# Kernel optimization log

Measured on AMD Instinct MI355X. Metric: run time of the kernel, lower is better.

Reference implementation:

```python
import jax, jax.numpy as jnp
import numpy as np

B, S, D = 2, 2048, 1024
H, HD = 16, 64  # head_dim = D // H
NEG = -9.0e15


def setup_inputs() -> dict:
    key = jax.random.key(0)
    ks = jax.random.split(key, 6)
    # xavier-uniform-like init for projections
    lim_qkv = float(np.sqrt(6.0 / (D + 3 * D)))
    lim_o = float(np.sqrt(6.0 / (D + D)))
    x = jax.random.normal(ks[0], (B, S, D), dtype=jnp.float32)
    qkv_w = jax.random.uniform(ks[1], (3 * D, D), minval=-lim_qkv, maxval=lim_qkv, dtype=jnp.float32)
    qkv_b = jnp.zeros((3 * D,), dtype=jnp.float32)
    o_w = jax.random.uniform(ks[2], (D, D), minval=-lim_o, maxval=lim_o, dtype=jnp.float32)
    o_b = jnp.zeros((D,), dtype=jnp.float32)
    # per-head thresholds ~ Uniform(0, 2/S): mean softmax prob is 1/S, so
    # roughly half the heads prune aggressively, half keep most entries.
    thresholds = jax.random.uniform(ks[3], (H,), dtype=jnp.float32) * (2.0 / S)
    return {"x": x, "thresholds": thresholds, "qkv_w": qkv_w, "qkv_b": qkv_b,
            "o_w": o_w, "o_b": o_b}


def reference(x, thresholds, qkv_w, qkv_b, o_w, o_b):
    # qkv projection: [B,S,3D] -> [B,S,H,3*HD] -> [B,H,S,3*HD]
    qkv = jnp.einsum('bsd,ed->bse', x, qkv_w) + qkv_b
    qkv = qkv.reshape(B, S, H, 3 * HD).transpose(0, 2, 1, 3)
    q, k, v = jnp.split(qkv, 3, axis=-1)  # each [B,H,S,HD]

    scale = 1.0 / jnp.sqrt(jnp.asarray(HD, dtype=q.dtype))
    attn_logits = jnp.einsum('bhqd,bhkd->bhqk', q, k) * scale  # [B,H,S,S]

    # first softmax only to build threshold mask (per-head threshold)
    att1 = jax.nn.softmax(attn_logits, axis=-1)
    mask = att1 > thresholds[None, :, None, None]

    # second, masked softmax
    masked_logits = jnp.where(mask, attn_logits, jnp.asarray(NEG, attn_logits.dtype))
    attention = jax.nn.softmax(masked_logits, axis=-1)

    values = jnp.einsum('bhqk,bhkd->bhqd', attention, v)  # [B,H,S,HD]
    values = values.transpose(0, 2, 1, 3).reshape(B, S, D)
    o = jnp.einsum('bsd,ed->bse', values, o_w) + o_b
    return o
```

## Files before the change

kernel.cpp:

```cpp
#include <hip/hip_runtime.h>
#include <math.h>

#define BATCH 2
#define S_LEN 2048
#define DMODEL 1024
#define NH 16
#define HDIM 64
#define SCALE 0.125f
#define KC 0.18033688011112042f

typedef short bf16x8 __attribute__((ext_vector_type(8)));
typedef _Float16 f16x8 __attribute__((ext_vector_type(8)));
typedef float f32x4 __attribute__((ext_vector_type(4)));
typedef unsigned short u16;
typedef unsigned short u16x4 __attribute__((ext_vector_type(4)));
#define MFMA(a, b, c) __builtin_amdgcn_mfma_f32_16x16x32_bf16(a, b, c, 0, 0, 0)
#define MFMA16(a, b, c) __builtin_amdgcn_mfma_f32_16x16x32_f16(a, b, c, 0, 0, 0)

static __device__ __forceinline__ float bf2f(u16 u) {
  return __uint_as_float(((unsigned int)u) << 16);
}
static __device__ __forceinline__ u16 f2h_bits(float a) {
  _Float16 h = (_Float16)a;
  return *(u16*)&h;
}

static __device__ __forceinline__ void split_bf16(float a, u16& hi, u16& lo) {
  unsigned int u = __float_as_uint(a);
  unsigned int r = (u + 0x7fffu + ((u >> 16) & 1u)) >> 16;
  hi = (u16)r;
  float res = a - __uint_as_float(r << 16);
  unsigned int u2 = __float_as_uint(res);
  lo = (u16)((u2 + 0x7fffu + ((u2 >> 16) & 1u)) >> 16);
}

static __device__ __forceinline__ float qredsum(float v) {
#pragma unroll
  for (int off = 8; off >= 1; off >>= 1) v += __shfl_xor(v, off, 16);
  return v;
}

static __device__ __forceinline__ void async_ld16(u16* lds, const u16* g) {
  __builtin_amdgcn_global_load_lds(
      (const __attribute__((address_space(1))) void*)(const void*)g,
      (__attribute__((address_space(3))) void*)(void*)lds, 16, 0, 0);
}

__global__ __launch_bounds__(256) void split_pair_kernel(
    const float* __restrict__ in, u16* __restrict__ hi, u16* __restrict__ lo,
    int n) {
  int idx = (blockIdx.x * 256 + threadIdx.x) * 4;
  if (idx >= n) return;
  float4 v = *(const float4*)(in + idx);
  u16 h0, h1, h2, h3, l0, l1, l2, l3;
  split_bf16(v.x, h0, l0);
  split_bf16(v.y, h1, l1);
  split_bf16(v.z, h2, l2);
  split_bf16(v.w, h3, l3);
  u16x4 h = {h0, h1, h2, h3};
  u16x4 l = {l0, l1, l2, l3};
  *(u16x4*)(hi + idx) = h;
  *(u16x4*)(lo + idx) = l;
}

__global__ __launch_bounds__(256) void qkv_gemm_mfma(
    const u16* __restrict__ xh, const u16* __restrict__ xl,
    const u16* __restrict__ wh, const u16* __restrict__ wl,
    const float* __restrict__ bias, u16* __restrict__ Qhi,
    u16* __restrict__ Qlo, u16* __restrict__ Khi, u16* __restrict__ Klo,
    u16* __restrict__ Vt) {
  __shared__ __align__(16) u16 Ah[4096], Al[4096], Bh[4096], Bl[4096];
  const int tid = threadIdx.x;
  const int w = tid >> 6, lane = tid & 63;
  const int m = lane & 15, quad = lane >> 4;
  const int wm = w >> 1, wn = w & 1;
  const int m0 = blockIdx.x * 128, n0 = blockIdx.y * 128;
  const int rl = lane >> 2, bp = lane & 3;
  const int sst = (rl >> 1) & 3;
  const int sa = (quad ^ ((m >> 1) & 3)) * 8;

  f32x4 acc[4][4];
  const f32x4 vzero = {0.f, 0.f, 0.f, 0.f};
#pragma unroll
  for (int mt = 0; mt < 4; ++mt)
#pragma unroll
    for (int nt = 0; nt < 4; ++nt) acc[mt][nt] = vzero;

  for (int k0 = 0; k0 < DMODEL; k0 += 32) {
#pragma unroll
    for (int i = 0; i < 2; ++i) {
      int cc = w * 2 + i;
      int row = cc * 16 + rl;
      int gofs = k0 + ((bp ^ sst) << 3);
      async_ld16(&Ah[cc * 512], xh + (size_t)(m0 + row) * DMODEL + gofs);
      async_ld16(&Al[cc * 512], xl + (size_t)(m0 + row) * DMODEL + gofs);
      async_ld16(&Bh[cc * 512], wh + (size_t)(n0 + row) * DMODEL + gofs);
      async_ld16(&Bl[cc * 512], wl + (size_t)(n0 + row) * DMODEL + gofs);
    }
    __syncthreads();
    bf16x8 afh[4], afl[4], bfh[4], bfl[4];
#pragma unroll
    for (int t = 0; t < 4; ++t) {
      int ra = (wm * 64 + t * 16 + m) * 32 + sa;
      afh[t] = *(const bf16x8*)&Ah[ra];
      afl[t] = *(const bf16x8*)&Al[ra];
      int rb = (wn * 64 + t * 16 + m) * 32 + sa;
      bfh[t] = *(const bf16x8*)&Bh[rb];
      bfl[t] = *(const bf16x8*)&Bl[rb];
    }
#pragma unroll
    for (int mt = 0; mt < 4; ++mt)
#pragma unroll
      for (int nt = 0; nt < 4; ++nt) {
        acc[mt][nt] = MFMA(afh[mt], bfh[nt], acc[mt][nt]);
        acc[mt][nt] = MFMA(afh[mt], bfl[nt], acc[mt][nt]);
        acc[mt][nt] = MFMA(afl[mt], bfh[nt], acc[mt][nt]);
      }
    __syncthreads();
  }
#pragma unroll
  for (int mt = 0; mt < 4; ++mt) {
#pragma unroll
    for (int rg = 0; rg < 4; ++rg) {
      int grow = m0 + wm * 64 + mt * 16 + quad * 4 + rg;
      int bb = grow >> 11, s = grow & (S_LEN - 1);
#pragma unroll
      for (int nt = 0; nt < 4; ++nt) {
        int e = n0 + wn * 64 + nt * 16 + m;
        float val = acc[mt][nt][rg] + bias[e];
        int h = e / 192;
        int r = e - h * 192;
        int d = r & 63;
        int bh = bb * NH + h;
        if (r < 64) {
          u16 hi, lo;
          split_bf16(val, hi, lo);
          int off = (bh * S_LEN + s) * HDIM + d;
          Qhi[off] = hi; Qlo[off] = lo;
        } else if (r < 128) {
          u16 hi, lo;
          split_bf16(val, hi, lo);
          int off = (bh * S_LEN + s) * HDIM + d;
          Khi[off] = hi; Klo[off] = lo;
        } else {
          Vt[(bh * HDIM + d) * S_LEN + s] = f2h_bits(val);
        }
      }
    }
  }
}

__global__ __launch_bounds__(256) void o_gemm_mfma(
    const u16* __restrict__ valh, const u16* __restrict__ vall,
    const float* __restrict__ ow, const float* __restrict__ bias,
    float* __restrict__ out) {
  __shared__ __align__(16) u16 Ah[4096], Al[4096], Bh[4096], Bl[4096];
  const int tid = threadIdx.x;
  const int w = tid >> 6, lane = tid & 63;
  const int m = lane & 15, quad = lane >> 4;
  const int wm = w >> 1, wn = w & 1;
  const int m0 = blockIdx.x * 128, n0 = blockIdx.y * 128;
  const int rl = lane >> 2, bp = lane & 3;
  const int sst = (rl >> 1) & 3;
  const int sa = (quad ^ ((m >> 1) & 3)) * 8;
  const int rB = tid >> 1, hf = tid & 1;
  const int sB = (rB >> 1) & 3;

  f32x4 acc[4][4];
  const f32x4 vzero = {0.f, 0.f, 0.f, 0.f};
#pragma unroll
  for (int mt = 0; mt < 4; ++mt)
#pragma unroll
    for (int nt = 0; nt < 4; ++nt) acc[mt][nt] = vzero;

  for (int k0 = 0; k0 < DMODEL; k0 += 32) {
#pragma unroll
    for (int i = 0; i < 2; ++i) {
      int cc = w * 2 + i;
      int row = cc * 16 + rl;
      int gofs = k0 + ((bp ^ sst) << 3);
      async_ld16(&Ah[cc * 512], valh + (size_t)(m0 + row) * DMODEL + gofs);
      async_ld16(&Al[cc * 512], vall + (size_t)(m0 + row) * DMODEL + gofs);
    }
    {
      const float* src = ow + (size_t)(n0 + rB) * DMODEL + k0 + hf * 16;
      float tmp[16];
      *(float4*)&tmp[0] = *(const float4*)(src);
      *(float4*)&tmp[4] = *(const float4*)(src + 4);
      *(float4*)&tmp[8] = *(const float4*)(src + 8);
      *(float4*)&tmp[12] = *(const float4*)(src + 12);
      u16 hbuf[16], lbuf[16];
#pragma unroll
      for (int ii = 0; ii < 16; ++ii) split_bf16(tmp[ii], hbuf[ii], lbuf[ii]);
#pragma unroll
      for (int j = 0; j < 2; ++j) {
        int bs = ((2 * hf + j) ^ sB) * 8;
        bf16x8 hv, lv;
#pragma unroll
        for (int q2 = 0; q2 < 8; ++q2) {
          hv[q2] = (short)hbuf[j * 8 + q2];
          lv[q2] = (short)lbuf[j * 8 + q2];
        }
        *(bf16x8*)&Bh[rB * 32 + bs] = hv;
        *(bf16x8*)&Bl[rB * 32 + bs] = lv;
      }
    }
    __syncthreads();
    bf16x8 afh[4], afl[4], bfh[4], bfl[4];
#pragma unroll
    for (int t = 0; t < 4; ++t) {
      int ra = (wm * 64 + t * 16 + m) * 32 + sa;
      afh[t] = *(const bf16x8*)&Ah[ra];
      afl[t] = *(const bf16x8*)&Al[ra];
      int rb = (wn * 64 + t * 16 + m) * 32 + sa;
      bfh[t] = *(const bf16x8*)&Bh[rb];
      bfl[t] = *(const bf16x8*)&Bl[rb];
    }
#pragma unroll
    for (int mt = 0; mt < 4; ++mt)
#pragma unroll
      for (int nt = 0; nt < 4; ++nt) {
        acc[mt][nt] = MFMA(afh[mt], bfh[nt], acc[mt][nt]);
        acc[mt][nt] = MFMA(afh[mt], bfl[nt], acc[mt][nt]);
        acc[mt][nt] = MFMA(afl[mt], bfh[nt], acc[mt][nt]);
      }
    __syncthreads();
  }
#pragma unroll
  for (int mt = 0; mt < 4; ++mt) {
#pragma unroll
    for (int rg = 0; rg < 4; ++rg) {
      int grow = m0 + wm * 64 + mt * 16 + quad * 4 + rg;
#pragma unroll
      for (int nt = 0; nt < 4; ++nt) {
        int e = n0 + wn * 64 + nt * 16 + m;
        out[(size_t)grow * DMODEL + e] = acc[mt][nt][rg] + bias[e];
      }
    }
  }
}

__global__ __launch_bounds__(256) void vsum_kernel(const u16* __restrict__ Vt,
                                                   float* __restrict__ vsum) {
  const int bh = blockIdx.x;
  const int tid = threadIdx.x;
  const int d = tid >> 2, part = tid & 3;
  int base = (bh * HDIM + d) * S_LEN + part * 512;
  float s = 0.f;
  for (int k = 0; k < 512; k += 8) {
    f16x8 vv = *(const f16x8*)(Vt + base + k);
#pragma unroll
    for (int j = 0; j < 8; ++j) s += (float)vv[j];
  }
  __shared__ float red[64][4];
  red[d][part] = s;
  __syncthreads();
  if (part == 0)
    vsum[bh * HDIM + d] = red[d][0] + red[d][1] + red[d][2] + red[d][3];
}

__global__ __launch_bounds__(256) void attn_mfma_kernel(
    const u16* __restrict__ Qhi, const u16* __restrict__ Qlo,
    const u16* __restrict__ Khi, const u16* __restrict__ Klo,
    const u16* __restrict__ Vt, const float* __restrict__ thr,
    const float* __restrict__ vsum, u16* __restrict__ valh,
    u16* __restrict__ vall) {
  const int blk = blockIdx.x;
  const int qt = blk & 31, bh = blk >> 5;
  const int h = bh & (NH - 1), bb = bh >> 4;
  const int tid = threadIdx.x;
  const int w = tid >> 6, lane = tid & 63;
  const int m = lane & 15, quad = lane >> 4;
  const int rsub = lane >> 3;
  const int bsw = (lane & 7) ^ rsub;

  __shared__ __align__(16) u16 Kh_s[2][4096];
  __shared__ __align__(16) u16 Kl_s[2][4096];
  __shared__ __align__(16) u16 Vs_s[4096];
  __shared__ __align__(16) u16 Pf_s[4][16][64];

  const int qoff = (bh * S_LEN + qt * 64 + w * 16 + m) * HDIM + quad * 8;
  const bf16x8 aQh0 = *(const bf16x8*)(Qhi + qoff);
  const bf16x8 aQh1 = *(const bf16x8*)(Qhi + qoff + 32);
  const bf16x8 aQl0 = *(const bf16x8*)(Qlo + qoff);
  const bf16x8 aQl1 = *(const bf16x8*)(Qlo + qoff + 32);

  const u16* KhT = Khi + bh * S_LEN * HDIM;
  const u16* KlT = Klo + bh * S_LEN * HDIM;
  const u16* VtT = Vt + bh * HDIM * S_LEN;
  const float th = thr[h];

  const int s0 = (quad ^ (m & 7)) * 8;
  const int s1 = ((4 + quad) ^ (m & 7)) * 8;

  float Zr[4], Z2r[4], tzr[4];
#pragma unroll
  for (int r = 0; r < 4; ++r) { Zr[r] = 0.f; Z2r[r] = 0.f; }

  const f32x4 vzero = {0.f, 0.f, 0.f, 0.f};

#define STAGE_K(bufi, t)                                                     \
  {                                                                          \
    const u16* gh = KhT + (t) * 64 * 64;                                     \
    const u16* gl = KlT + (t) * 64 * 64;                                     \
    _Pragma("unroll") for (int i = 0; i < 2; ++i) {                          \
      int c = w * 2 + i;                                                     \
      int row = c * 8 + rsub;                                                \
      async_ld16(&Kh_s[bufi][c * 512], gh + row * 64 + bsw * 8);             \
      async_ld16(&Kl_s[bufi][c * 512], gl + row * 64 + bsw * 8);             \
    }                                                                        \
  }
#define STAGE_V(t)                                                           \
  {                                                                          \
    _Pragma("unroll") for (int i = 0; i < 2; ++i) {                          \
      int c = w * 2 + i;                                                     \
      int row = c * 8 + rsub;                                                \
      async_ld16(&Vs_s[c * 512], VtT + row * 2048 + (t) * 64 + bsw * 8);     \
    }                                                                        \
  }

#define QK_TILE(cur)                                                         \
  _Pragma("unroll") for (int nt = 0; nt < 4; ++nt) {                         \
    const int ro = (nt * 16 + m) * 64;                                       \
    bf16x8 kh0 = *(const bf16x8*)&Kh_s[cur][ro + s0];                        \
    bf16x8 kh1 = *(const bf16x8*)&Kh_s[cur][ro + s1];                        \
    bf16x8 kl0 = *(const bf16x8*)&Kl_s[cur][ro + s0];                        \
    bf16x8 kl1 = *(const bf16x8*)&Kl_s[cur][ro + s1];                        \
    acc[nt] = MFMA(aQh0, kh0, acc[nt]);                                      \
    acc[nt] = MFMA(aQh1, kh1, acc[nt]);                                      \
    acc[nt] = MFMA(aQh0, kl0, acc[nt]);                                      \
    acc[nt] = MFMA(aQh1, kl1, acc[nt]);                                      \
    acc[nt] = MFMA(aQl0, kh0, acc[nt]);                                      \
    acc[nt] = MFMA(aQl1, kh1, acc[nt]);                                      \
  }

  STAGE_K(0, 0);
  __syncthreads();
  for (int t = 0; t < 32; ++t) {
    const int cur = t & 1;
    if (t < 31) STAGE_K(cur ^ 1, t + 1);
    f32x4 acc[4];
#pragma unroll
    for (int nt = 0; nt < 4; ++nt) acc[nt] = vzero;
    QK_TILE(cur);
#pragma unroll
    for (int r = 0; r < 4; ++r) {
      Zr[r] += __builtin_exp2f(acc[0][r] * KC) + __builtin_exp2f(acc[1][r] * KC) +
               __builtin_exp2f(acc[2][r] * KC) + __builtin_exp2f(acc[3][r] * KC);
    }
    __syncthreads();
  }
#pragma unroll
  for (int r = 0; r < 4; ++r) tzr[r] = th * qredsum(Zr[r]);

  f32x4 oacc[4];
#pragma unroll
  for (int nt = 0; nt < 4; ++nt) oacc[nt] = vzero;

  STAGE_K(0, 0);
  __syncthreads();
  for (int t = 0; t < 32; ++t) {
    const int cur = t & 1;
    STAGE_V(t);
    if (t < 31) STAGE_K(cur ^ 1, t + 1);
    f32x4 acc[4];
#pragma unroll
    for (int nt = 0; nt < 4; ++nt) acc[nt] = vzero;
    QK_TILE(cur);
#pragma unroll
    for (int r = 0; r < 4; ++r) {
      int row = quad * 4 + r;
      float psum = 0.f;
#pragma unroll
      for (int nt = 0; nt < 4; ++nt) {
        float pu = __builtin_exp2f(acc[nt][r] * KC);
        float p = (pu > tzr[r]) ? pu : 0.f;
        _Float16 p16 = (_Float16)p;
        psum += (float)p16;
        int col = nt * 16 + m;
        int cs = (((col >> 3) ^ (row & 7)) << 3) | (col & 7);
        Pf_s[w][row][cs] = *(u16*)&p16;
      }
      Z2r[r] += psum;
    }
    __syncthreads();
    f16x8 aP0 = *(const f16x8*)&Pf_s[w][m][s0];
    f16x8 aP1 = *(const f16x8*)&Pf_s[w][m][s1];
#pragma unroll
    for (int nt = 0; nt < 4; ++nt) {
      const int ro = (nt * 16 + m) * 64;
      f16x8 vv0 = *(const f16x8*)&Vs_s[ro + s0];
      f16x8 vv1 = *(const f16x8*)&Vs_s[ro + s1];
      oacc[nt] = MFMA16(aP0, vv0, oacc[nt]);
      oacc[nt] = MFMA16(aP1, vv1, oacc[nt]);
    }
    __syncthreads();
  }

#pragma unroll
  for (int r = 0; r < 4; ++r) {
    float z2 = qredsum(Z2r[r]);
    float invz = (z2 > 0.f) ? (1.f / z2) : 0.f;
    int srow = qt * 64 + w * 16 + quad * 4 + r;
#pragma unroll
    for (int nt = 0; nt < 4; ++nt) {
      float vs = vsum[bh * HDIM + nt * 16 + m];
      float o = (z2 > 0.f) ? (oacc[nt][r] * invz) : (vs * (1.0f / S_LEN));
      int idx = (bb * S_LEN + srow) * DMODEL + h * HDIM + nt * 16 + m;
      u16 hi, lo;
      split_bf16(o, hi, lo);
      valh[idx] = hi;
      vall[idx] = lo;
    }
  }
}

extern "C" void kernel_launch(void* const* d_in, const int* in_sizes, int n_in,
                              void* d_out, int out_size, void* d_ws, size_t ws_size,
                              hipStream_t stream) {
  const float* x = (const float*)d_in[0];
  const float* thresholds = (const float*)d_in[1];
  const float* qkv_w = (const float*)d_in[2];
  const float* qkv_b = (const float*)d_in[3];
  const float* o_w = (const float*)d_in[4];
  const float* o_b = (const float*)d_in[5];

  const size_t NBH = (size_t)BATCH * NH * S_LEN * HDIM;
  u16* base = (u16*)d_ws;
  u16* Qhi = base;
  u16* Qlo = base + NBH;
  u16* Khi = base + 2 * NBH;
  u16* Klo = base + 3 * NBH;
  u16* Vt = base + 4 * NBH;
  float* vsum = (float*)(base + 5 * NBH);
  u16* R1 = (u16*)(vsum + 2048);
  u16* xh = R1;
  u16* xl = R1 + NBH;
  u16* valh = R1;
  u16* vall = R1 + NBH;
  u16* wh = (u16*)d_out;
  u16* wl = wh + (size_t)3 * DMODEL * DMODEL;

  split_pair_kernel<<<4096, 256, 0, stream>>>(x, xh, xl, (int)NBH);
  split_pair_kernel<<<3072, 256, 0, stream>>>(qkv_w, wh, wl, 3 * DMODEL * DMODEL);
  dim3 g1(32, 24);
  qkv_gemm_mfma<<<g1, 256, 0, stream>>>(xh, xl, wh, wl, qkv_b, Qhi, Qlo, Khi,
                                        Klo, Vt);
  vsum_kernel<<<BATCH * NH, 256, 0, stream>>>(Vt, vsum);
  attn_mfma_kernel<<<BATCH * NH * (S_LEN / 64), 256, 0, stream>>>(
      Qhi, Qlo, Khi, Klo, Vt, thresholds, vsum, valh, vall);
  dim3 g3(32, 8);
  o_gemm_mfma<<<g3, 256, 0, stream>>>(valh, vall, o_w, o_b, (float*)d_out);
}
```

Measured before the change: 437.2 us.

## Split K hi/lo staging in attention and merge split kernels into one launch

The attention kernel now double-buffers only the K-hi tile and loads the K-lo tile into a single buffer each iteration, issuing the hi MFMAs before a barrier and the lo MFMAs after it. The old barrier between the P store and the P·V step is removed and its role is taken by the new mid-tile barrier. This cuts LDS use, which could raise occupancy, but it exposes the K-lo load latency inside each iteration. The two fp32-to-bf16 split launches for x and the QKV weights are also merged into one kernel to save a launch.

```diff
diff --git a/kernel.cpp b/kernel.cpp
--- a/kernel.cpp
+++ b/kernel.cpp
@@ -46,11 +46,9 @@
       (__attribute__((address_space(3))) void*)(void*)lds, 16, 0, 0);
 }
 
-__global__ __launch_bounds__(256) void split_pair_kernel(
-    const float* __restrict__ in, u16* __restrict__ hi, u16* __restrict__ lo,
-    int n) {
-  int idx = (blockIdx.x * 256 + threadIdx.x) * 4;
-  if (idx >= n) return;
+static __device__ __forceinline__ void do_split4(const float* __restrict__ in,
+                                                 u16* __restrict__ hi,
+                                                 u16* __restrict__ lo, int idx) {
   float4 v = *(const float4*)(in + idx);
   u16 h0, h1, h2, h3, l0, l1, l2, l3;
   split_bf16(v.x, h0, l0);
@@ -61,6 +59,19 @@
   u16x4 l = {l0, l1, l2, l3};
   *(u16x4*)(hi + idx) = h;
   *(u16x4*)(lo + idx) = l;
+}
+
+__global__ __launch_bounds__(256) void split_two_kernel(
+    const float* __restrict__ a, u16* __restrict__ ah, u16* __restrict__ al,
+    int na, const float* __restrict__ b, u16* __restrict__ bh,
+    u16* __restrict__ bl, int nb) {
+  int idx = (blockIdx.x * 256 + threadIdx.x) * 4;
+  if (idx < na) {
+    do_split4(a, ah, al, idx);
+  } else {
+    int j = idx - na;
+    if (j < nb) do_split4(b, bh, bl, j);
+  }
 }
 
 __global__ __launch_bounds__(256) void qkv_gemm_mfma(
@@ -275,7 +286,7 @@
   const int bsw = (lane & 7) ^ rsub;
 
   __shared__ __align__(16) u16 Kh_s[2][4096];
-  __shared__ __align__(16) u16 Kl_s[2][4096];
+  __shared__ __align__(16) u16 Kl_s[4096];
   __shared__ __align__(16) u16 Vs_s[4096];
   __shared__ __align__(16) u16 Pf_s[4][16][64];
 
@@ -299,15 +310,22 @@
 
   const f32x4 vzero = {0.f, 0.f, 0.f, 0.f};
 
-#define STAGE_K(bufi, t)                                                     \
+#define STAGE_KH(bufi, t)                                                    \
   {                                                                          \
     const u16* gh = KhT + (t) * 64 * 64;                                     \
+    _Pragma("unroll") for (int i = 0; i < 2; ++i) {                          \
+      int c = w * 2 + i;                                                     \
+      int row = c * 8 + rsub;                                                \
+      async_ld16(&Kh_s[bufi][c * 512], gh + row * 64 + bsw * 8);             \
+    }                                                                        \
+  }
+#define STAGE_KL(t)                                                          \
+  {                                                                          \
     const u16* gl = KlT + (t) * 64 * 64;                                     \
     _Pragma("unroll") for (int i = 0; i < 2; ++i) {                          \
       int c = w * 2 + i;                                                     \
       int row = c * 8 + rsub;                                                \
-      async_ld16(&Kh_s[bufi][c * 512], gh + row * 64 + bsw * 8);             \
-      async_ld16(&Kl_s[bufi][c * 512], gl + row * 64 + bsw * 8);             \
+      async_ld16(&Kl_s[c * 512], gl + row * 64 + bsw * 8);                   \
     }                                                                        \
   }
 #define STAGE_V(t)                                                           \
@@ -319,30 +337,37 @@
     }                                                                        \
   }
 
-#define QK_TILE(cur)                                                         \
+#define QK_HI(cur)                                                           \
   _Pragma("unroll") for (int nt = 0; nt < 4; ++nt) {                         \
     const int ro = (nt * 16 + m) * 64;                                       \
     bf16x8 kh0 = *(const bf16x8*)&Kh_s[cur][ro + s0];                        \
     bf16x8 kh1 = *(const bf16x8*)&Kh_s[cur][ro + s1];                        \
-    bf16x8 kl0 = *(const bf16x8*)&Kl_s[cur][ro + s0];                        \
-    bf16x8 kl1 = *(const bf16x8*)&Kl_s[cur][ro + s1];                        \
     acc[nt] = MFMA(aQh0, kh0, acc[nt]);                                      \
     acc[nt] = MFMA(aQh1, kh1, acc[nt]);                                      \
+    acc[nt] = MFMA(aQl0, kh0, acc[nt]);                                      \
+    acc[nt] = MFMA(aQl1, kh1, acc[nt]);                                      \
+  }
+#define QK_LO()                                                              \
+  _Pragma("unroll") for (int nt = 0; nt < 4; ++nt) {                         \
+    const int ro = (nt * 16 + m) * 64;                                       \
+    bf16x8 kl0 = *(const bf16x8*)&Kl_s[ro + s0];                             \
+    bf16x8 kl1 = *(const bf16x8*)&Kl_s[ro + s1];                             \
     acc[nt] = MFMA(aQh0, kl0, acc[nt]);                                      \
     acc[nt] = MFMA(aQh1, kl1, acc[nt]);                                      \
-    acc[nt] = MFMA(aQl0, kh0, acc[nt]);                                      \
-    acc[nt] = MFMA(aQl1, kh1, acc[nt]);                                      \
-  }
-
-  STAGE_K(0, 0);
+  }
+
+  STAGE_KH(0, 0);
   __syncthreads();
   for (int t = 0; t < 32; ++t) {
     const int cur = t & 1;
-    if (t < 31) STAGE_K(cur ^ 1, t + 1);
+    STAGE_KL(t);
+    if (t < 31) STAGE_KH(cur ^ 1, t + 1);
     f32x4 acc[4];
 #pragma unroll
     for (int nt = 0; nt < 4; ++nt) acc[nt] = vzero;
-    QK_TILE(cur);
+    QK_HI(cur);
+    __syncthreads();
+    QK_LO();
 #pragma unroll
     for (int r = 0; r < 4; ++r) {
       Zr[r] += __builtin_exp2f(acc[0][r] * KC) + __builtin_exp2f(acc[1][r] * KC) +
@@ -357,16 +382,19 @@
 #pragma unroll
   for (int nt = 0; nt < 4; ++nt) oacc[nt] = vzero;
 
-  STAGE_K(0, 0);
+  STAGE_KH(0, 0);
   __syncthreads();
   for (int t = 0; t < 32; ++t) {
     const int cur = t & 1;
+    STAGE_KL(t);
     STAGE_V(t);
-    if (t < 31) STAGE_K(cur ^ 1, t + 1);
+    if (t < 31) STAGE_KH(cur ^ 1, t + 1);
     f32x4 acc[4];
 #pragma unroll
     for (int nt = 0; nt < 4; ++nt) acc[nt] = vzero;
-    QK_TILE(cur);
+    QK_HI(cur);
+    __syncthreads();
+    QK_LO();
 #pragma unroll
     for (int r = 0; r < 4; ++r) {
       int row = quad * 4 + r;
@@ -383,7 +411,6 @@
       }
       Z2r[r] += psum;
     }
-    __syncthreads();
     f16x8 aP0 = *(const f16x8*)&Pf_s[w][m][s0];
     f16x8 aP1 = *(const f16x8*)&Pf_s[w][m][s1];
 #pragma unroll
@@ -426,6 +453,7 @@
   const float* o_b = (const float*)d_in[5];
 
   const size_t NBH = (size_t)BATCH * NH * S_LEN * HDIM;
+  const int NW = 3 * DMODEL * DMODEL;
   u16* base = (u16*)d_ws;
   u16* Qhi = base;
   u16* Qlo = base + NBH;
@@ -439,10 +467,11 @@
   u16* valh = R1;
   u16* vall = R1 + NBH;
   u16* wh = (u16*)d_out;
-  u16* wl = wh + (size_t)3 * DMODEL * DMODEL;
-
-  split_pair_kernel<<<4096, 256, 0, stream>>>(x, xh, xl, (int)NBH);
-  split_pair_kernel<<<3072, 256, 0, stream>>>(qkv_w, wh, wl, 3 * DMODEL * DMODEL);
+  u16* wl = wh + (size_t)NW;
+
+  int ntot = ((int)NBH + NW) / 4;
+  split_two_kernel<<<(ntot + 255) / 256, 256, 0, stream>>>(
+      x, xh, xl, (int)NBH, qkv_w, wh, wl, NW);
   dim3 g1(32, 24);
   qkv_gemm_mfma<<<g1, 256, 0, stream>>>(xh, xl, wh, wl, qkv_b, Qhi, Qlo, Khi,
                                         Klo, Vt);
```

Result: no change. 436.8 us (-0.1%).
